# Performance work log

Measured on AMD Instinct MI355X. Metric: run time of the kernel, lower is better.

The kernel has to match this reference:

```python
import jax, jax.numpy as jnp
import numpy as np

B, P, S, E, H, NC, NR, NL = 32, 1024, 128, 768, 8, 5, 3, 3


def _adjacency():
    adj = np.zeros((NC, NC, NR), dtype=np.float32)
    for i, j in [(0, 1), (0, 2), (1, 2), (2, 3)]:  # co-occurrence (symmetric)
        adj[i, j, 0] = 1.0
        adj[j, i, 0] = 1.0
    adj[3, 2, 1] = 1.0  # hierarchical
    for i in range(NC):  # self loops
        adj[i, i, 2] = 1.0
    return jnp.asarray(adj)


def _ln(x, g, b, eps=1e-5):
    m = x.mean(-1, keepdims=True)
    v = ((x - m) ** 2).mean(-1, keepdims=True)
    return (x - m) * jax.lax.rsqrt(v + eps) * g + b


def _mha(q, k, v, Wqkv, bqkv, Wo, bo, h=H):
    # torch nn.MultiheadAttention, batch_first=True, eval mode (no dropout),
    # returns (output, attn weights averaged over heads)
    Bq, Lq, Eq = q.shape
    Lk = k.shape[1]
    d = Eq // h
    Wq, Wk, Wv = jnp.split(Wqkv, 3, axis=0)
    bq, bk, bv = jnp.split(bqkv, 3, axis=0)
    qh = (q @ Wq.T + bq).reshape(Bq, Lq, h, d).transpose(0, 2, 1, 3)
    kh = (k @ Wk.T + bk).reshape(Bq, Lk, h, d).transpose(0, 2, 1, 3)
    vh = (v @ Wv.T + bv).reshape(Bq, Lk, h, d).transpose(0, 2, 1, 3)
    scores = jnp.einsum('bhqd,bhkd->bhqk', qh, kh) / jnp.sqrt(jnp.asarray(d, q.dtype))
    a = jax.nn.softmax(scores, axis=-1)
    o = jnp.einsum('bhqk,bhkd->bhqd', a, vh).transpose(0, 2, 1, 3).reshape(Bq, Lq, Eq)
    return o @ Wo.T + bo, a.mean(axis=1)


def setup_inputs() -> dict:
    key = jax.random.key(0)
    ks = iter(jax.random.split(key, 64))
    n = lambda *s: jax.random.normal(next(ks), s, dtype=jnp.float32) * 0.02
    return {
        'visual_features': jax.random.normal(next(ks), (B, P, E), dtype=jnp.float32),
        'text_features': jax.random.normal(next(ks), (B, S, E), dtype=jnp.float32),
        'sentence_embedding': jax.random.normal(next(ks), (B, E), dtype=jnp.float32),
        'class_presence': (jax.random.uniform(next(ks), (B, NC)) > 0.5).astype(jnp.float32),
        # graph layer params stacked over NL layers
        'g_node_emb': n(NL, NC, E), 'g_edge_emb': n(NL, NR, E),
        'g_Wqkv': n(NL, 3 * E, E), 'g_bqkv': jnp.zeros((NL, 3 * E)),
        'g_Wo': n(NL, E, E), 'g_bo': jnp.zeros((NL, E)),
        'g_W1': n(NL, E, 2 * E), 'g_b1': jnp.zeros((NL, E)),
        'g_lng': jnp.ones((NL, E)), 'g_lnb': jnp.zeros((NL, E)),
        'g_W2': n(NL, E, E), 'g_b2': jnp.zeros((NL, E)),
        # visual-text fusion MHA
        'v_Wqkv': n(3 * E, E), 'v_bqkv': jnp.zeros((3 * E,)),
        'v_Wo': n(E, E), 'v_bo': jnp.zeros((E,)),
        # per-class feature generators stacked over NC classes
        'c_W1': n(NC, E, E), 'c_b1': jnp.zeros((NC, E)),
        'c_lng': jnp.ones((NC, E)), 'c_lnb': jnp.zeros((NC, E)),
        'c_W2': n(NC, E, E), 'c_b2': jnp.zeros((NC, E)),
        # global fusion MLP
        'gf_W1': n(E, 2 * E), 'gf_b1': jnp.zeros((E,)),
        'gf_lng': jnp.ones((E,)), 'gf_lnb': jnp.zeros((E,)),
        'gf_W2': n(E, E), 'gf_b2': jnp.zeros((E,)),
        # output proj + final norm
        'out_W': n(E, E), 'out_b': jnp.zeros((E,)),
        'norm_g': jnp.ones((E,)), 'norm_b': jnp.zeros((E,)),
    }


def reference(visual_features, text_features, sentence_embedding, class_presence,
              g_node_emb, g_edge_emb, g_Wqkv, g_bqkv, g_Wo, g_bo, g_W1, g_b1,
              g_lng, g_lnb, g_W2, g_b2, v_Wqkv, v_bqkv, v_Wo, v_bo,
              c_W1, c_b1, c_lng, c_lnb, c_W2, c_b2,
              gf_W1, gf_b1, gf_lng, gf_lnb, gf_W2, gf_b2,
              out_W, out_b, norm_g, norm_b):
    adj = _adjacency()
    Bc = visual_features.shape[0]
    sent = sentence_embedding
    activated, scores = None, None
    for l in range(NL):  # small fixed layer loop
        node_emb = g_node_emb[l]  # [NC, E]
        # sum over relation types of (adj_r @ node_emb) * edge_emb_r, / NR
        edge_feat = jnp.einsum('ijr,je,re->ie', adj, node_emb, g_edge_emb[l]) / NR
        node_f = jnp.broadcast_to(node_emb, (Bc, NC, E))
        combined = jnp.concatenate([node_f, jnp.broadcast_to(edge_feat, (Bc, NC, E))], axis=-1)
        h = combined @ g_W1[l].T + g_b1[l]
        h = jax.nn.relu(_ln(h, g_lng[l], g_lnb[l]))
        updated = h @ g_W2[l].T + g_b2[l]  # [B, NC, E]
        _, w = _mha(sent[:, None, :], updated, updated, g_Wqkv[l], g_bqkv[l], g_Wo[l], g_bo[l])
        scores = jax.nn.softmax(w[:, 0, :] * (class_presence + 0.1), axis=-1)
        activated = updated * scores[..., None]
        sent = sent + activated.mean(axis=1)
    fused, _ = _mha(visual_features, text_features, text_features, v_Wqkv, v_bqkv, v_Wo, v_bo)
    grounded = _ln(visual_features + fused, norm_g, norm_b)
    # grouped per-class MLPs (batched over classes via einsum)
    cf = jnp.einsum('bce,cfe->bcf', activated, c_W1) + c_b1
    cf = jax.nn.relu(_ln(cf, c_lng, c_lnb))
    cf = jnp.einsum('bce,cfe->bcf', cf, c_W2) + c_b2
    gc = jnp.broadcast_to(sent[:, None, :], (Bc, NC, E))
    g = jnp.concatenate([cf, gc], axis=-1) @ gf_W1.T + gf_b1
    g = jax.nn.relu(_ln(g, gf_lng, gf_lnb))
    class_guidance = g @ gf_W2.T + gf_b2
    grounded_out = grounded @ out_W.T + out_b
    return grounded_out, class_guidance, scores
```

## Files before the change

### kernel.cpp

```cpp
#include <hip/hip_runtime.h>
#include <stdint.h>

typedef unsigned short u16;
typedef __attribute__((ext_vector_type(8))) short short8;
typedef __attribute__((ext_vector_type(4))) float f32x4;

#define NB 32
#define PP 1024
#define SEQ 128
#define EE 768
#define HH 8
#define DD 96
#define NCC 5
#define NLL 3

__device__ __forceinline__ float bf2f(u16 x){ unsigned u=((unsigned)x)<<16; float f; __builtin_memcpy(&f,&u,4); return f; }
__device__ __forceinline__ u16 f2bf(float f){ unsigned u; __builtin_memcpy(&u,&f,4); u=(u+0x7FFFu+((u>>16)&1u))>>16; return (u16)u; }

__device__ __forceinline__ short8 cvt8(const float* p) {
  f32x4 a = *(const f32x4*)p;
  f32x4 b = *(const f32x4*)(p+4);
  short8 r;
  r[0]=(short)f2bf(a[0]); r[1]=(short)f2bf(a[1]); r[2]=(short)f2bf(a[2]); r[3]=(short)f2bf(a[3]);
  r[4]=(short)f2bf(b[0]); r[5]=(short)f2bf(b[1]); r[6]=(short)f2bf(b[2]); r[7]=(short)f2bf(b[3]);
  return r;
}

__device__ __forceinline__ void gl16(const u16* g, u16* l) {
  __builtin_amdgcn_global_load_lds((const __attribute__((address_space(1))) void*)g,
                                   (__attribute__((address_space(3))) void*)l, 16, 0, 0);
}

__global__ __launch_bounds__(256) void k_cvt(const float* __restrict__ s, u16* __restrict__ d, int n8) {
  int i = blockIdx.x*256 + threadIdx.x;
  const int stride = gridDim.x*256;
  for (; i < n8; i += stride) *(short8*)(d + (size_t)i*8) = cvt8(s + (size_t)i*8);
}

__device__ __forceinline__ void ln_stats(float v0, float v1, float v2, float* red, int t,
                                         float& mean, float& rstd) {
  float ps = v0+v1+v2;
  float ps2 = v0*v0+v1*v1+v2*v2;
  #pragma unroll
  for (int o=32;o;o>>=1){ ps += __shfl_down(ps,o,64); ps2 += __shfl_down(ps2,o,64); }
  if ((t&63)==0){ red[t>>6]=ps; red[4+(t>>6)]=ps2; }
  __syncthreads();
  mean = (red[0]+red[1]+red[2]+red[3])*(1.0f/EE);
  float var = (red[4]+red[5]+red[6]+red[7])*(1.0f/EE) - mean*mean;
  rstd = rsqrtf(var + 1e-5f);
  __syncthreads();
}

template<int EPI>
__global__ __launch_bounds__(256) void gemm_bt(const u16* __restrict__ A, const u16* __restrict__ Bw,
        const float* __restrict__ bias, const u16* __restrict__ Res,
        u16* __restrict__ C, float* __restrict__ Cf, u16* __restrict__ C2, int M, int N, int K)
{
  __shared__ u16 As[2][4096];
  __shared__ u16 Bs[2][4096];
  const int m0 = blockIdx.x*128, n0 = blockIdx.y*128;
  const int t = threadIdx.x;
  const int lane = t&63, w = t>>6, wr = w>>1, wc = w&1, lm = lane&15, lg = lane>>4;
  const int o   = w*1024 + lane*16;
  const int srow = o>>6;
  const int sg   = ((o>>4)&3) ^ ((srow>>1)&3);
  const u16* ag = A  + (size_t)(m0+srow)*K + sg*8;
  const u16* bg = Bw + (size_t)(n0+srow)*K + sg*8;
  const size_t rstep = (size_t)64*K;
  const int s  = (lm>>1)&3;
  const int ra = (wr*64+lm)*32 + (lg^s)*8;
  const int rb = (wc*64+lm)*32 + (lg^s)*8;

  f32x4 acc[4][4] = {};
  gl16(ag,         &As[0][w*512]);
  gl16(ag + rstep, &As[0][2048 + w*512]);
  gl16(bg,         &Bs[0][w*512]);
  gl16(bg + rstep, &Bs[0][2048 + w*512]);
  __syncthreads();
  int cur = 0;
  const int NT = K>>5;
  for (int kt=0; kt<NT; ++kt) {
    if (kt+1 < NT) {
      const int k0 = (kt+1)<<5;
      gl16(ag + k0,         &As[cur^1][w*512]);
      gl16(ag + k0 + rstep, &As[cur^1][2048 + w*512]);
      gl16(bg + k0,         &Bs[cur^1][w*512]);
      gl16(bg + k0 + rstep, &Bs[cur^1][2048 + w*512]);
    }
    short8 af[4], bf[4];
    #pragma unroll
    for (int mi=0;mi<4;mi++) af[mi] = *(const short8*)&As[cur][ra + mi*512];
    #pragma unroll
    for (int ni=0;ni<4;ni++) bf[ni] = *(const short8*)&Bs[cur][rb + ni*512];
    #pragma unroll
    for (int mi=0;mi<4;mi++)
      #pragma unroll
      for (int ni=0;ni<4;ni++)
        acc[mi][ni] = __builtin_amdgcn_mfma_f32_16x16x32_bf16(af[mi], bf[ni], acc[mi][ni], 0,0,0);
    __syncthreads();
    cur ^= 1;
  }
  #pragma unroll
  for (int mi=0;mi<4;mi++) {
    #pragma unroll
    for (int ni=0;ni<4;ni++) {
      const int col = n0 + wc*64 + ni*16 + lm;
      const float bv = bias[col];
      #pragma unroll
      for (int r=0;r<4;r++) {
        const int row = m0 + wr*64 + mi*16 + lg*4 + r;
        float v = acc[mi][ni][r] + bv;
        if constexpr (EPI==1) v += bf2f(Res[(size_t)row*N + col]);
        if constexpr (EPI==3) {
          Cf[(size_t)row*N + col] = v;
        } else if constexpr (EPI==2) {
          if (col < EE) C[(size_t)row*EE + col] = f2bf(v);
          else C2[((size_t)(row>>7)*EE + (col-EE))*SEQ + (row&127)] = f2bf(v);
        } else {
          C[(size_t)row*N + col] = f2bf(v);
        }
      }
    }
  }
}

template<int MT, int AF>
__global__ __launch_bounds__(256) void gemm_tk(const void* __restrict__ Av, const float* __restrict__ W,
    float* __restrict__ Ppart, int ngroups, int KS, int K, int lda, long strideA, long strideW)
{
  const int task = blockIdx.x;
  const int nt = task % 6;
  const int g  = (task/6) % ngroups;
  const int ks = task/(6*ngroups);
  const int t = threadIdx.x, l = t&63, w = t>>6, lm = l&15, lg = l>>4;
  const int slice = K/KS, kbase = ks*slice;
  const int n0 = nt*128 + w*32;
  W += (size_t)g*strideW;
  f32x4 acc[MT/16][2] = {};
  for (int ki=0; ki<slice; ki+=32) {
    const int k0 = kbase + ki;
    short8 af[MT/16];
    #pragma unroll
    for (int m=0;m<MT/16;m++) {
      if constexpr (AF) af[m] = cvt8((const float*)Av + (size_t)g*strideA + (size_t)(m*16+lm)*lda + k0 + lg*8);
      else af[m] = *(const short8*)((const u16*)Av + (size_t)g*strideA + (size_t)(m*16+lm)*lda + k0 + lg*8);
    }
    #pragma unroll
    for (int ni=0;ni<2;ni++) {
      const short8 bf = cvt8(W + (size_t)(n0+ni*16+lm)*K + k0 + lg*8);
      #pragma unroll
      for (int m=0;m<MT/16;m++)
        acc[m][ni] = __builtin_amdgcn_mfma_f32_16x16x32_bf16(af[m], bf, acc[m][ni], 0,0,0);
    }
  }
  float* pb = Ppart + (size_t)(ks*ngroups+g)*MT*768;
  #pragma unroll
  for (int m=0;m<MT/16;m++)
    #pragma unroll
    for (int ni=0;ni<2;ni++)
      #pragma unroll
      for (int r=0;r<4;r++)
        pb[(size_t)(m*16+lg*4+r)*768 + n0+ni*16+lm] = acc[m][ni][r];
}

__global__ __launch_bounds__(256) void k_red(const float* __restrict__ Ppart,
    float* __restrict__ outF, u16* __restrict__ outB,
    const float* __restrict__ bias, long strideB,
    int MT, int ngroups, int KS, int Mreal, long strideR, long strideG)
{
  const int bid = blockIdx.x, g = bid/Mreal, rr = bid%Mreal, t = threadIdx.x;
  #pragma unroll
  for (int i=0;i<3;i++) {
    const int e = t + i*256;
    float s = bias[(size_t)g*strideB + e];
    for (int ks=0; ks<KS; ++ks) s += Ppart[((size_t)(ks*ngroups+g)*MT + rr)*768 + e];
    const size_t off = (size_t)rr*strideR + (size_t)g*strideG + e;
    if (outF) outF[off] = s;
    if (outB) outB[off] = f2bf(s);
  }
}

__global__ __launch_bounds__(256) void k_lnred(const float* __restrict__ Ppart, u16* __restrict__ out,
    const float* __restrict__ bias, long strideB,
    const float* __restrict__ gamma, const float* __restrict__ beta, long strideLn,
    int MT, int ngroups, int KS, int Mreal, long strideR, long strideG)
{
  const int bid = blockIdx.x, g = bid/Mreal, rr = bid%Mreal, t = threadIdx.x;
  __shared__ float red[8];
  float v[3];
  #pragma unroll
  for (int i=0;i<3;i++) {
    const int e = t + i*256;
    float s = bias[(size_t)g*strideB + e];
    for (int ks=0; ks<KS; ++ks) s += Ppart[((size_t)(ks*ngroups+g)*MT + rr)*768 + e];
    v[i] = s;
  }
  float mean, rstd;
  ln_stats(v[0],v[1],v[2], red, t, mean, rstd);
  #pragma unroll
  for (int i=0;i<3;i++) {
    const int e = t + i*256;
    out[(size_t)rr*strideR + (size_t)g*strideG + e] =
        f2bf(fmaxf((v[i]-mean)*rstd*gamma[(size_t)g*strideLn+e]+beta[(size_t)g*strideLn+e], 0.f));
  }
}

__global__ __launch_bounds__(256) void k_comb(const float* __restrict__ node_all,
    const float* __restrict__ edge_all, u16* __restrict__ comb)
{
  const int lc = blockIdx.x, ll = lc/NCC, c = lc%NCC, t = threadIdx.x;
  const float* node = node_all + (size_t)ll*NCC*EE;
  const float* edge = edge_all + (size_t)ll*3*EE;
  #pragma unroll
  for (int i=0;i<3;i++) {
    const int e = t + i*256;
    float n0=node[e], n1=node[EE+e], n2=node[2*EE+e], n3=node[3*EE+e];
    float nc_=node[(size_t)c*EE+e];
    float e0=edge[e], e1=edge[EE+e], e2=edge[2*EE+e];
    float s0;
    if (c==0) s0=n1+n2; else if (c==1) s0=n0+n2; else if (c==2) s0=n0+n1+n3; else if (c==3) s0=n2; else s0=0.f;
    float ef = (s0*e0 + ((c==3)? n2*e1 : 0.f) + nc_*e2)*(1.0f/3.0f);
    comb[(size_t)lc*2*EE + e]      = f2bf(nc_);
    comb[(size_t)lc*2*EE + EE + e] = f2bf(ef);
  }
}

__global__ __launch_bounds__(256) void k_sent_init(const float* __restrict__ se, float* __restrict__ sent) {
  const int i = blockIdx.x*256 + threadIdx.x;
  if (i < NB*EE) sent[i] = se[i];
}

__global__ __launch_bounds__(256) void k_attn2(int l, const float* __restrict__ qpart,
    const float* __restrict__ bq,
    const float* __restrict__ presence, const float* __restrict__ upd, const float* __restrict__ khg,
    float* __restrict__ sent, float* __restrict__ sc_ws, float* __restrict__ out_scores)
{
  const int b = blockIdx.x, t = threadIdx.x;
  __shared__ float qh[EE];
  __shared__ float scl[HH][NCC];
  __shared__ float wsc[NCC];
  __shared__ float scr[NCC];
  #pragma unroll
  for (int i=0;i<3;i++) {
    const int e = t + i*256;
    float s = bq[e];
    #pragma unroll
    for (int ks=0; ks<8; ++ks) s += qpart[((size_t)ks*NB + b)*768 + e];
    qh[e] = s;
  }
  __syncthreads();
  if (t < HH*NCC) {
    const int hh=t/NCC, cc=t%NCC;
    const float* kr = khg + (size_t)(l*NCC+cc)*EE + hh*DD;
    float a=0.f;
    #pragma unroll 8
    for (int d=0;d<DD;d++) a += qh[hh*DD+d]*kr[d];
    scl[hh][cc]=a*0.1020620726159658f;
  }
  __syncthreads();
  if (t < HH) {
    float m=scl[t][0];
    #pragma unroll
    for (int c2=1;c2<NCC;c2++) m=fmaxf(m,scl[t][c2]);
    float ex[NCC]; float s=0.f;
    #pragma unroll
    for (int c2=0;c2<NCC;c2++){ ex[c2]=__expf(scl[t][c2]-m); s+=ex[c2]; }
    #pragma unroll
    for (int c2=0;c2<NCC;c2++) scl[t][c2]=ex[c2]/s;
  }
  __syncthreads();
  if (t < NCC) {
    float wv=0.f;
    #pragma unroll
    for (int hh=0;hh<HH;hh++) wv += scl[hh][t];
    wv *= (1.0f/HH);
    wsc[t] = wv*(presence[b*NCC+t]+0.1f);
  }
  __syncthreads();
  if (t==0) {
    float m=wsc[0];
    #pragma unroll
    for (int c2=1;c2<NCC;c2++) m=fmaxf(m,wsc[c2]);
    float ex[NCC]; float s=0.f;
    #pragma unroll
    for (int c2=0;c2<NCC;c2++){ ex[c2]=__expf(wsc[c2]-m); s+=ex[c2]; }
    #pragma unroll
    for (int c2=0;c2<NCC;c2++){
      float v=ex[c2]/s; scr[c2]=v; sc_ws[b*NCC+c2]=v;
      if (out_scores) out_scores[b*NCC+c2]=v;
    }
  }
  __syncthreads();
  #pragma unroll
  for (int i=0;i<3;i++) {
    const int e=t+i*256;
    float a=0.f;
    #pragma unroll
    for (int c2=0;c2<NCC;c2++) a += scr[c2]*upd[(size_t)(l*NCC+c2)*EE+e];
    sent[(size_t)b*EE+e] += a*(1.0f/NCC);
  }
}

__global__ __launch_bounds__(256) void k_actprep(const float* __restrict__ upd, const float* __restrict__ sc_ws,
    const float* __restrict__ sent, u16* __restrict__ actB, u16* __restrict__ cat)
{
  const int bid = blockIdx.x, c = bid/NB, b = bid%NB, t = threadIdx.x;
  const float sc = sc_ws[b*NCC+c];
  #pragma unroll
  for (int i=0;i<3;i++) {
    const int e = t + i*256;
    actB[((size_t)c*NB + b)*EE + e] = f2bf(upd[(size_t)(2*NCC+c)*EE + e]*sc);
    cat[((size_t)(b*NCC+c))*2*EE + EE + e] = f2bf(sent[(size_t)b*EE + e]);
  }
}

__global__ __launch_bounds__(256) void attn_k(u16* __restrict__ Q, const u16* __restrict__ Kb,
                                              const u16* __restrict__ Vt)
{
  const int qt = blockIdx.x, h = blockIdx.y, b = blockIdx.z;
  const int t = threadIdx.x, l = t&63, w = t>>6, wr = w>>1, wc = w&1, lm = l&15, lg = l>>4;
  __shared__ u16 Ps[64][136];
  __shared__ float redm[2][64];
  __shared__ float reds[2][64];
  u16* qb = Q + ((size_t)(b*PP + qt*64))*EE + h*DD;
  const u16* kb = Kb + ((size_t)b*SEQ)*EE + h*DD;
  const u16* vb = Vt + ((size_t)(b*HH+h))*DD*SEQ;

  f32x4 acc[2][4] = {};
  #pragma unroll
  for (int kc=0;kc<3;kc++) {
    short8 af[2], bv[4];
    #pragma unroll
    for (int mi=0;mi<2;mi++) af[mi] = *(const short8*)(qb + (size_t)(wr*32+mi*16+lm)*EE + kc*32 + lg*8);
    #pragma unroll
    for (int ni=0;ni<4;ni++) bv[ni] = *(const short8*)(kb + (size_t)(wc*64+ni*16+lm)*EE + kc*32 + lg*8);
    #pragma unroll
    for (int mi=0;mi<2;mi++)
      #pragma unroll
      for (int ni=0;ni<4;ni++)
        acc[mi][ni] = __builtin_amdgcn_mfma_f32_16x16x32_bf16(af[mi], bv[ni], acc[mi][ni], 0,0,0);
  }
  const float scale = 0.1020620726159658f;
  float gmax[2][4], gsum[2][4];
  #pragma unroll
  for (int mi=0;mi<2;mi++)
    #pragma unroll
    for (int r=0;r<4;r++) {
      float v = fmaxf(fmaxf(acc[mi][0][r],acc[mi][1][r]),fmaxf(acc[mi][2][r],acc[mi][3][r]));
      #pragma unroll
      for (int mk=1;mk<16;mk<<=1) v = fmaxf(v, __shfl_xor(v,mk,64));
      gmax[mi][r]=v;
    }
  if (lm==0) {
    #pragma unroll
    for (int mi=0;mi<2;mi++)
      #pragma unroll
      for (int r=0;r<4;r++) redm[wc][wr*32+mi*16+lg*4+r] = gmax[mi][r];
  }
  __syncthreads();
  #pragma unroll
  for (int mi=0;mi<2;mi++)
    #pragma unroll
    for (int r=0;r<4;r++) {
      const int row = wr*32+mi*16+lg*4+r;
      gmax[mi][r] = fmaxf(redm[0][row], redm[1][row]);
    }
  #pragma unroll
  for (int mi=0;mi<2;mi++)
    #pragma unroll
    for (int r=0;r<4;r++) {
      float s=0.f;
      #pragma unroll
      for (int ni=0;ni<4;ni++) {
        float p = __expf((acc[mi][ni][r]-gmax[mi][r])*scale);
        acc[mi][ni][r]=p; s+=p;
      }
      #pragma unroll
      for (int mk=1;mk<16;mk<<=1) s += __shfl_xor(s,mk,64);
      gsum[mi][r]=s;
    }
  __syncthreads();
  if (lm==0) {
    #pragma unroll
    for (int mi=0;mi<2;mi++)
      #pragma unroll
      for (int r=0;r<4;r++) reds[wc][wr*32+mi*16+lg*4+r] = gsum[mi][r];
  }
  __syncthreads();
  #pragma unroll
  for (int mi=0;mi<2;mi++)
    #pragma unroll
    for (int r=0;r<4;r++) {
      const int row = wr*32+mi*16+lg*4+r;
      const float inv = 1.0f/(reds[0][row]+reds[1][row]);
      #pragma unroll
      for (int ni=0;ni<4;ni++)
        Ps[row][wc*64+ni*16+lm] = f2bf(acc[mi][ni][r]*inv);
    }
  __syncthreads();

  f32x4 oacc[2][3] = {};
  #pragma unroll
  for (int kc=0;kc<4;kc++) {
    short8 pa[2], vv[3];
    #pragma unroll
    for (int mi=0;mi<2;mi++) pa[mi] = *(const short8*)&Ps[wr*32+mi*16+lm][kc*32+lg*8];
    #pragma unroll
    for (int ni=0;ni<3;ni++) vv[ni] = *(const short8*)(vb + (size_t)(wc*48+ni*16+lm)*SEQ + kc*32 + lg*8);
    #pragma unroll
    for (int mi=0;mi<2;mi++)
      #pragma unroll
      for (int ni=0;ni<3;ni++)
        oacc[mi][ni] = __builtin_amdgcn_mfma_f32_16x16x32_bf16(pa[mi], vv[ni], oacc[mi][ni], 0,0,0);
  }
  #pragma unroll
  for (int mi=0;mi<2;mi++)
    #pragma unroll
    for (int ni=0;ni<3;ni++)
      #pragma unroll
      for (int r=0;r<4;r++)
        qb[(size_t)(wr*32+mi*16+lg*4+r)*EE + wc*48+ni*16+lm] = f2bf(oacc[mi][ni][r]);
}

__global__ __launch_bounds__(256) void k_ln(u16* __restrict__ G, const float* __restrict__ gw, const float* __restrict__ gb)
{
  const int row = blockIdx.x, t = threadIdx.x;
  u16* p = G + (size_t)row*EE;
  __shared__ float red[8];
  float v[3];
  #pragma unroll
  for (int i=0;i<3;i++) v[i]=bf2f(p[t+i*256]);
  float mean, rstd;
  ln_stats(v[0],v[1],v[2], red, t, mean, rstd);
  #pragma unroll
  for (int i=0;i<3;i++) {
    const int e=t+i*256;
    p[e]=f2bf((v[i]-mean)*rstd*gw[e]+gb[e]);
  }
}

extern "C" void kernel_launch(void* const* d_in, const int* in_sizes, int n_in,
                              void* d_out, int out_size, void* d_ws, size_t ws_size,
                              hipStream_t stream)
{
  const float* visual   = (const float*)d_in[0];
  const float* text     = (const float*)d_in[1];
  const float* sentemb  = (const float*)d_in[2];
  const float* presence = (const float*)d_in[3];
  const float* gnode = (const float*)d_in[4];
  const float* gedge = (const float*)d_in[5];
  const float* gWqkv = (const float*)d_in[6];
  const float* gbqkv = (const float*)d_in[7];
  const float* gW1 = (const float*)d_in[10];
  const float* gb1 = (const float*)d_in[11];
  const float* glng = (const float*)d_in[12];
  const float* glnb = (const float*)d_in[13];
  const float* gW2 = (const float*)d_in[14];
  const float* gb2 = (const float*)d_in[15];
  const float* vWqkv = (const float*)d_in[16];
  const float* vbqkv = (const float*)d_in[17];
  const float* vWo = (const float*)d_in[18];
  const float* vbo = (const float*)d_in[19];
  const float* cW1 = (const float*)d_in[20];
  const float* cb1 = (const float*)d_in[21];
  const float* clng = (const float*)d_in[22];
  const float* clnb = (const float*)d_in[23];
  const float* cW2 = (const float*)d_in[24];
  const float* cb2 = (const float*)d_in[25];
  const float* gfW1 = (const float*)d_in[26];
  const float* gfb1 = (const float*)d_in[27];
  const float* gflng = (const float*)d_in[28];
  const float* gflnb = (const float*)d_in[29];
  const float* gfW2 = (const float*)d_in[30];
  const float* gfb2 = (const float*)d_in[31];
  const float* outW = (const float*)d_in[32];
  const float* outb = (const float*)d_in[33];
  const float* normg = (const float*)d_in[34];
  const float* normb = (const float*)d_in[35];

  char* ws = (char*)d_ws;
  u16* wsG   = (u16*)(ws);
  u16* wsK   = (u16*)(ws + 50331648);
  u16* wsVt  = (u16*)(ws + 56623104);
  u16* visB  = (u16*)(ws + 62914560);
  u16* outWB = wsK;

  char* dob = (char*)d_out;
  u16* wsQ    = (u16*)(dob);
  u16* textB  = (u16*)(dob + 50331648);
  u16* WqkvB  = (u16*)(dob + 56623104);
  u16* WoB    = (u16*)(dob + 60162048);
  char* P = dob + 61341696;
  float* wsSent   = (float*)(P);
  float* wsUpd    = (float*)(P +   98304);
  float* wsKhg    = (float*)(P +  144384);
  float* wsScores = (float*)(P +  190464);
  u16*   wsComb   = (u16*)  (P +  191104);
  u16*   wsHb     = (u16*)  (P +  237184);
  u16*   wsUpdB   = (u16*)  (P +  260224);
  u16*   wsActB   = (u16*)  (P +  283264);
  u16*   wsH1b    = (u16*)  (P +  529024);
  u16*   wsCat    = (u16*)  (P +  774784);
  u16*   wsG1b    = (u16*)  (P + 1266304);
  float* Ppart    = (float*)(P + 1512064);

  float* outGO = (float*)d_out;
  float* outCG = outGO + 25165824;
  float* outSC = outGO + 25288704;

  k_cvt<<<dim3(2048), dim3(256), 0, stream>>>(visual, visB, 3145728);
  k_cvt<<<dim3(1024), dim3(256), 0, stream>>>(text, textB, 393216);
  k_cvt<<<dim3(512),  dim3(256), 0, stream>>>(vWqkv, WqkvB, 221184);
  k_cvt<<<dim3(512),  dim3(256), 0, stream>>>(vWo, WoB, 73728);

  k_comb<<<dim3(NLL*NCC), dim3(256), 0, stream>>>(gnode, gedge, wsComb);
  gemm_tk<16,0><<<dim3(144), dim3(256), 0, stream>>>(wsComb, gW1, Ppart,
      3, 8, 2*EE, 2*EE, (long)NCC*2*EE, (long)EE*2*EE);
  k_lnred<<<dim3(15), dim3(256), 0, stream>>>(Ppart, wsHb, gb1, EE, glng, glnb, EE,
      16, 3, 8, 5, 768, 3840);
  gemm_tk<16,0><<<dim3(72), dim3(256), 0, stream>>>(wsHb, gW2, Ppart,
      3, 4, EE, EE, (long)NCC*EE, (long)EE*EE);
  k_red<<<dim3(15), dim3(256), 0, stream>>>(Ppart, wsUpd, wsUpdB, gb2, EE,
      16, 3, 4, 5, 768, 3840);
  gemm_tk<16,0><<<dim3(72), dim3(256), 0, stream>>>(wsUpdB, gWqkv + (size_t)EE*EE, Ppart,
      3, 4, EE, EE, (long)NCC*EE, (long)3*EE*EE);
  k_red<<<dim3(15), dim3(256), 0, stream>>>(Ppart, wsKhg, nullptr, gbqkv + EE, (long)3*EE,
      16, 3, 4, 5, 768, 3840);

  k_sent_init<<<dim3(96), dim3(256), 0, stream>>>(sentemb, wsSent);
  for (int l=0;l<NLL;l++) {
    gemm_tk<32,1><<<dim3(48), dim3(256), 0, stream>>>(wsSent, gWqkv + (size_t)l*3*EE*EE, Ppart,
        1, 8, EE, EE, 0, 0);
    k_attn2<<<dim3(NB), dim3(256), 0, stream>>>(l, Ppart, gbqkv + (size_t)l*3*EE,
        presence, wsUpd, wsKhg, wsSent, wsScores, (l==NLL-1)?outSC:(float*)nullptr);
  }

  k_actprep<<<dim3(NCC*NB), dim3(256), 0, stream>>>(wsUpd, wsScores, wsSent, wsActB, wsCat);
  gemm_tk<32,0><<<dim3(120), dim3(256), 0, stream>>>(wsActB, cW1, Ppart,
      5, 4, EE, EE, (long)NB*EE, (long)EE*EE);
  k_lnred<<<dim3(160), dim3(256), 0, stream>>>(Ppart, wsH1b, cb1, EE, clng, clnb, EE,
      32, 5, 4, 32, 768, 24576);
  gemm_tk<32,0><<<dim3(120), dim3(256), 0, stream>>>(wsH1b, cW2, Ppart,
      5, 4, EE, EE, (long)NB*EE, (long)EE*EE);
  k_red<<<dim3(160), dim3(256), 0, stream>>>(Ppart, nullptr, wsCat, cb2, EE,
      32, 5, 4, 32, 7680, 1536);
  gemm_tk<32,0><<<dim3(120), dim3(256), 0, stream>>>(wsCat, gfW1, Ppart,
      5, 4, 2*EE, 2*EE, (long)NB*2*EE, 0);
  k_lnred<<<dim3(160), dim3(256), 0, stream>>>(Ppart, wsG1b, gfb1, 0, gflng, gflnb, 0,
      32, 5, 4, 32, 768, 24576);
  gemm_tk<32,0><<<dim3(120), dim3(256), 0, stream>>>(wsG1b, gfW2, Ppart,
      5, 4, EE, EE, (long)NB*EE, 0);
  k_red<<<dim3(160), dim3(256), 0, stream>>>(Ppart, outCG, nullptr, gfb2, 0,
      32, 5, 4, 32, 768, 24576);

  gemm_bt<0><<<dim3(256,6), dim3(256), 0, stream>>>(visB, WqkvB, vbqkv, nullptr,
                                                    wsQ, nullptr, nullptr, NB*PP, EE, EE);
  gemm_bt<2><<<dim3(32,12), dim3(256), 0, stream>>>(textB, WqkvB + (size_t)EE*EE, vbqkv+EE, nullptr,
                                                    wsK, nullptr, wsVt, NB*SEQ, 2*EE, EE);
  attn_k<<<dim3(PP/64, HH, NB), dim3(256), 0, stream>>>(wsQ, wsK, wsVt);
  k_cvt<<<dim3(512), dim3(256), 0, stream>>>(outW, outWB, 73728);
  gemm_bt<1><<<dim3(256,6), dim3(256), 0, stream>>>(wsQ, WoB, vbo, visB,
                                                    wsG, nullptr, nullptr, NB*PP, EE, EE);
  k_ln<<<dim3(NB*PP), dim3(256), 0, stream>>>(wsG, normg, normb);
  gemm_bt<3><<<dim3(256,6), dim3(256), 0, stream>>>(wsG, outWB, outb, nullptr,
                                                    nullptr, outGO, nullptr, NB*PP, EE, EE);
}
```

Measured before the change: 483.7 us.

## Remap GEMM workgroups across XCDs and fuse small launch kernels

The large bf16 GEMMs now run on a 1D grid. Block IDs are remapped so that blocks placed round-robin on the 8 XCDs each take a contiguous run of tiles, all N tiles of an M row-block together, which aims to improve L2 reuse of A rows. Four conversion launches are merged into one kernel, sentence init is folded into the comb kernel, and the activation prep is fused into the last attention-layer kernel, cutting launch count. The remap assumes the grid size is divisible by 8, and the fused actprep adds per-thread serial stores in k_attn2.

```diff
diff --git a/kernel.cpp b/kernel.cpp
--- a/kernel.cpp
+++ b/kernel.cpp
@@ -31,6 +31,24 @@
                                    (__attribute__((address_space(3))) void*)l, 16, 0, 0);
 }
 
+__global__ __launch_bounds__(256) void k_cvt4(
+    const float* __restrict__ s0, u16* __restrict__ d0, int c0,
+    const float* __restrict__ s1, u16* __restrict__ d1, int c1,
+    const float* __restrict__ s2, u16* __restrict__ d2, int c2,
+    const float* __restrict__ s3, u16* __restrict__ d3, int c3)
+{
+  int i = blockIdx.x*256 + threadIdx.x;
+  const int stride = gridDim.x*256;
+  const int tot = c0+c1+c2+c3;
+  for (; i < tot; i += stride) {
+    int j = i; const float* s; u16* d;
+    if (j < c0) { s=s0; d=d0; }
+    else { j-=c0; if (j<c1){s=s1;d=d1;}
+      else { j-=c1; if (j<c2){s=s2;d=d2;} else { j-=c2; s=s3; d=d3; } } }
+    *(short8*)(d + (size_t)j*8) = cvt8(s + (size_t)j*8);
+  }
+}
+
 __global__ __launch_bounds__(256) void k_cvt(const float* __restrict__ s, u16* __restrict__ d, int n8) {
   int i = blockIdx.x*256 + threadIdx.x;
   const int stride = gridDim.x*256;
@@ -54,11 +72,15 @@
 template<int EPI>
 __global__ __launch_bounds__(256) void gemm_bt(const u16* __restrict__ A, const u16* __restrict__ Bw,
         const float* __restrict__ bias, const u16* __restrict__ Res,
-        u16* __restrict__ C, float* __restrict__ Cf, u16* __restrict__ C2, int M, int N, int K)
+        u16* __restrict__ C, float* __restrict__ Cf, u16* __restrict__ C2,
+        int M, int N, int K, int NTB)
 {
   __shared__ u16 As[2][4096];
   __shared__ u16 Bs[2][4096];
-  const int m0 = blockIdx.x*128, n0 = blockIdx.y*128;
+  const int nwg = gridDim.x;
+  const int bid = blockIdx.x;
+  const int task = (bid & 7)*(nwg >> 3) + (bid >> 3);
+  const int m0 = (task / NTB)*128, n0 = (task % NTB)*128;
   const int t = threadIdx.x;
   const int lane = t&63, w = t>>6, wr = w>>1, wc = w&1, lm = lane&15, lg = lane>>4;
   const int o   = w*1024 + lane*16;
@@ -205,35 +227,38 @@
   }
 }
 
-__global__ __launch_bounds__(256) void k_comb(const float* __restrict__ node_all,
-    const float* __restrict__ edge_all, u16* __restrict__ comb)
-{
-  const int lc = blockIdx.x, ll = lc/NCC, c = lc%NCC, t = threadIdx.x;
-  const float* node = node_all + (size_t)ll*NCC*EE;
-  const float* edge = edge_all + (size_t)ll*3*EE;
-  #pragma unroll
-  for (int i=0;i<3;i++) {
-    const int e = t + i*256;
-    float n0=node[e], n1=node[EE+e], n2=node[2*EE+e], n3=node[3*EE+e];
-    float nc_=node[(size_t)c*EE+e];
-    float e0=edge[e], e1=edge[EE+e], e2=edge[2*EE+e];
-    float s0;
-    if (c==0) s0=n1+n2; else if (c==1) s0=n0+n2; else if (c==2) s0=n0+n1+n3; else if (c==3) s0=n2; else s0=0.f;
-    float ef = (s0*e0 + ((c==3)? n2*e1 : 0.f) + nc_*e2)*(1.0f/3.0f);
-    comb[(size_t)lc*2*EE + e]      = f2bf(nc_);
-    comb[(size_t)lc*2*EE + EE + e] = f2bf(ef);
-  }
-}
-
-__global__ __launch_bounds__(256) void k_sent_init(const float* __restrict__ se, float* __restrict__ sent) {
-  const int i = blockIdx.x*256 + threadIdx.x;
-  if (i < NB*EE) sent[i] = se[i];
+__global__ __launch_bounds__(256) void k_comb_si(const float* __restrict__ node_all,
+    const float* __restrict__ edge_all, u16* __restrict__ comb,
+    const float* __restrict__ se, float* __restrict__ sent)
+{
+  const int bid = blockIdx.x, t = threadIdx.x;
+  if (bid < NLL*NCC) {
+    const int ll = bid/NCC, c = bid%NCC;
+    const float* node = node_all + (size_t)ll*NCC*EE;
+    const float* edge = edge_all + (size_t)ll*3*EE;
+    #pragma unroll
+    for (int i=0;i<3;i++) {
+      const int e = t + i*256;
+      float n0=node[e], n1=node[EE+e], n2=node[2*EE+e], n3=node[3*EE+e];
+      float nc_=node[(size_t)c*EE+e];
+      float e0=edge[e], e1=edge[EE+e], e2=edge[2*EE+e];
+      float s0;
+      if (c==0) s0=n1+n2; else if (c==1) s0=n0+n2; else if (c==2) s0=n0+n1+n3; else if (c==3) s0=n2; else s0=0.f;
+      float ef = (s0*e0 + ((c==3)? n2*e1 : 0.f) + nc_*e2)*(1.0f/3.0f);
+      comb[(size_t)bid*2*EE + e]      = f2bf(nc_);
+      comb[(size_t)bid*2*EE + EE + e] = f2bf(ef);
+    }
+  } else {
+    const int i = (bid - NLL*NCC)*256 + t;
+    if (i < NB*EE) sent[i] = se[i];
+  }
 }
 
 __global__ __launch_bounds__(256) void k_attn2(int l, const float* __restrict__ qpart,
     const float* __restrict__ bq,
     const float* __restrict__ presence, const float* __restrict__ upd, const float* __restrict__ khg,
-    float* __restrict__ sent, float* __restrict__ sc_ws, float* __restrict__ out_scores)
+    float* __restrict__ sent, float* __restrict__ sc_ws, float* __restrict__ out_scores,
+    u16* __restrict__ actB, u16* __restrict__ cat)
 {
   const int b = blockIdx.x, t = threadIdx.x;
   __shared__ float qh[EE];
@@ -297,20 +322,16 @@
     float a=0.f;
     #pragma unroll
     for (int c2=0;c2<NCC;c2++) a += scr[c2]*upd[(size_t)(l*NCC+c2)*EE+e];
-    sent[(size_t)b*EE+e] += a*(1.0f/NCC);
-  }
-}
-
-__global__ __launch_bounds__(256) void k_actprep(const float* __restrict__ upd, const float* __restrict__ sc_ws,
-    const float* __restrict__ sent, u16* __restrict__ actB, u16* __restrict__ cat)
-{
-  const int bid = blockIdx.x, c = bid/NB, b = bid%NB, t = threadIdx.x;
-  const float sc = sc_ws[b*NCC+c];
-  #pragma unroll
-  for (int i=0;i<3;i++) {
-    const int e = t + i*256;
-    actB[((size_t)c*NB + b)*EE + e] = f2bf(upd[(size_t)(2*NCC+c)*EE + e]*sc);
-    cat[((size_t)(b*NCC+c))*2*EE + EE + e] = f2bf(sent[(size_t)b*EE + e]);
+    const float sn = sent[(size_t)b*EE+e] + a*(1.0f/NCC);
+    sent[(size_t)b*EE+e] = sn;
+    if (out_scores) {
+      const u16 snb = f2bf(sn);
+      #pragma unroll
+      for (int c2=0;c2<NCC;c2++) {
+        actB[((size_t)c2*NB + b)*EE + e] = f2bf(upd[(size_t)(2*NCC+c2)*EE + e]*scr[c2]);
+        cat[((size_t)(b*NCC+c2))*2*EE + EE + e] = snb;
+      }
+    }
   }
 }
 
@@ -508,12 +529,12 @@
   float* outCG = outGO + 25165824;
   float* outSC = outGO + 25288704;
 
-  k_cvt<<<dim3(2048), dim3(256), 0, stream>>>(visual, visB, 3145728);
-  k_cvt<<<dim3(1024), dim3(256), 0, stream>>>(text, textB, 393216);
-  k_cvt<<<dim3(512),  dim3(256), 0, stream>>>(vWqkv, WqkvB, 221184);
-  k_cvt<<<dim3(512),  dim3(256), 0, stream>>>(vWo, WoB, 73728);
-
-  k_comb<<<dim3(NLL*NCC), dim3(256), 0, stream>>>(gnode, gedge, wsComb);
+  k_cvt4<<<dim3(2048), dim3(256), 0, stream>>>(visual, visB, 3145728,
+                                               text, textB, 393216,
+                                               vWqkv, WqkvB, 221184,
+                                               vWo, WoB, 73728);
+
+  k_comb_si<<<dim3(NLL*NCC + 96), dim3(256), 0, stream>>>(gnode, gedge, wsComb, sentemb, wsSent);
   gemm_tk<16,0><<<dim3(144), dim3(256), 0, stream>>>(wsComb, gW1, Ppart,
       3, 8, 2*EE, 2*EE, (long)NCC*2*EE, (long)EE*2*EE);
   k_lnred<<<dim3(15), dim3(256), 0, stream>>>(Ppart, wsHb, gb1, EE, glng, glnb, EE,
@@ -527,15 +548,14 @@
   k_red<<<dim3(15), dim3(256), 0, stream>>>(Ppart, wsKhg, nullptr, gbqkv + EE, (long)3*EE,
       16, 3, 4, 5, 768, 3840);
 
-  k_sent_init<<<dim3(96), dim3(256), 0, stream>>>(sentemb, wsSent);
   for (int l=0;l<NLL;l++) {
     gemm_tk<32,1><<<dim3(48), dim3(256), 0, stream>>>(wsSent, gWqkv + (size_t)l*3*EE*EE, Ppart,
         1, 8, EE, EE, 0, 0);
     k_attn2<<<dim3(NB), dim3(256), 0, stream>>>(l, Ppart, gbqkv + (size_t)l*3*EE,
-        presence, wsUpd, wsKhg, wsSent, wsScores, (l==NLL-1)?outSC:(float*)nullptr);
-  }
-
-  k_actprep<<<dim3(NCC*NB), dim3(256), 0, stream>>>(wsUpd, wsScores, wsSent, wsActB, wsCat);
+        presence, wsUpd, wsKhg, wsSent, wsScores,
+        (l==NLL-1)?outSC:(float*)nullptr, wsActB, wsCat);
+  }
+
   gemm_tk<32,0><<<dim3(120), dim3(256), 0, stream>>>(wsActB, cW1, Ppart,
       5, 4, EE, EE, (long)NB*EE, (long)EE*EE);
   k_lnred<<<dim3(160), dim3(256), 0, stream>>>(Ppart, wsH1b, cb1, EE, clng, clnb, EE,
@@ -553,15 +573,15 @@
   k_red<<<dim3(160), dim3(256), 0, stream>>>(Ppart, outCG, nullptr, gfb2, 0,
       32, 5, 4, 32, 768, 24576);
 
-  gemm_bt<0><<<dim3(256,6), dim3(256), 0, stream>>>(visB, WqkvB, vbqkv, nullptr,
-                                                    wsQ, nullptr, nullptr, NB*PP, EE, EE);
-  gemm_bt<2><<<dim3(32,12), dim3(256), 0, stream>>>(textB, WqkvB + (size_t)EE*EE, vbqkv+EE, nullptr,
-                                                    wsK, nullptr, wsVt, NB*SEQ, 2*EE, EE);
+  gemm_bt<0><<<dim3(1536), dim3(256), 0, stream>>>(visB, WqkvB, vbqkv, nullptr,
+                                                   wsQ, nullptr, nullptr, NB*PP, EE, EE, 6);
+  gemm_bt<2><<<dim3(384), dim3(256), 0, stream>>>(textB, WqkvB + (size_t)EE*EE, vbqkv+EE, nullptr,
+                                                  wsK, nullptr, wsVt, NB*SEQ, 2*EE, EE, 12);
   attn_k<<<dim3(PP/64, HH, NB), dim3(256), 0, stream>>>(wsQ, wsK, wsVt);
   k_cvt<<<dim3(512), dim3(256), 0, stream>>>(outW, outWB, 73728);
-  gemm_bt<1><<<dim3(256,6), dim3(256), 0, stream>>>(wsQ, WoB, vbo, visB,
-                                                    wsG, nullptr, nullptr, NB*PP, EE, EE);
+  gemm_bt<1><<<dim3(1536), dim3(256), 0, stream>>>(wsQ, WoB, vbo, visB,
+                                                   wsG, nullptr, nullptr, NB*PP, EE, EE, 6);
   k_ln<<<dim3(NB*PP), dim3(256), 0, stream>>>(wsG, normg, normb);
-  gemm_bt<3><<<dim3(256,6), dim3(256), 0, stream>>>(wsG, outWB, outb, nullptr,
-                                                    nullptr, outGO, nullptr, NB*PP, EE, EE);
-}
+  gemm_bt<3><<<dim3(1536), dim3(256), 0, stream>>>(wsG, outWB, outb, nullptr,
+                                                   nullptr, outGO, nullptr, NB*PP, EE, EE, 6);
+}
```

Measured after the change: 474.7 us. Within noise of the previous version (-1.9%).
